# Kernel optimization log

Measured on AMD Instinct MI355X. Metric: run time of the kernel, lower is better.

Reference implementation:

```python
import jax, jax.numpy as jnp
import numpy as np

IN_CHANNELS = 8
CHANNELS = 8
MASK_OUT_STRIDE = 4


def aligned_bilinear(x, factor):
    # Faithful port of AdelaiDet aligned_bilinear (align_corners=True).
    if factor == 1:
        return x
    n, c, h, w = x.shape
    x = jnp.pad(x, ((0, 0), (0, 0), (0, 1), (0, 1)), mode='edge')
    oh, ow = factor * h + 1, factor * w + 1

    def interp_axis(arr, out_len, axis):
        # align_corners=True from size s+1 -> factor*s+1: src coord = i / factor
        coords = jnp.arange(out_len) / factor
        i0 = jnp.floor(coords).astype(jnp.int32)
        i1 = jnp.minimum(i0 + 1, arr.shape[axis] - 1)
        t = (coords - i0).astype(arr.dtype)
        a0 = jnp.take(arr, i0, axis=axis)
        a1 = jnp.take(arr, i1, axis=axis)
        shp = [1] * arr.ndim
        shp[axis] = out_len
        t = t.reshape(shp)
        return a0 * (1 - t) + a1 * t

    x = interp_axis(x, oh, 2)
    x = interp_axis(x, ow, 3)
    p = factor // 2
    x = jnp.pad(x, ((0, 0), (0, 0), (p, 0), (p, 0)), mode='edge')
    return x[:, :, : oh - 1, : ow - 1]


def setup_inputs() -> dict:
    key = jax.random.key(0)
    ks = jax.random.split(key, 6)
    N, C, H, W = 4, IN_CHANNELS, 112, 200
    n_inst = 200
    stride = 8
    num_gen_params = (C + 2) * CHANNELS + CHANNELS + CHANNELS * CHANNELS + CHANNELS + CHANNELS + 1  # 169
    mask_feats = jax.random.normal(ks[0], (N, C, H, W), dtype=jnp.float32)
    mask_head_params = jax.random.normal(ks[1], (n_inst, num_gen_params), dtype=jnp.float32) * 0.1
    # instance centers anywhere inside the image (in input-image pixel coords)
    instance_locations = jax.random.uniform(ks[2], (n_inst, 2), dtype=jnp.float32) * jnp.array(
        [W * stride, H * stride], dtype=jnp.float32)
    sizes_of_interest = jnp.array([64.0, 128.0, 256.0, 512.0, 1024.0], dtype=jnp.float32)
    im_inds = jax.random.randint(ks[3], (n_inst,), 0, N, dtype=jnp.int32)
    fpn_levels = jax.random.randint(ks[4], (n_inst,), 0, 5, dtype=jnp.int32)
    return {
        'mask_feats': mask_feats,
        'mask_head_params': mask_head_params,
        'instance_locations': instance_locations,
        'sizes_of_interest': sizes_of_interest,
        'im_inds': im_inds,
        'fpn_levels': fpn_levels,
        'mask_feat_stride': stride,
    }


def reference(mask_feats, mask_head_params, instance_locations, sizes_of_interest,
              im_inds, fpn_levels, mask_feat_stride):
    N, C, H, W = mask_feats.shape
    n_inst = mask_head_params.shape[0]
    HW = H * W
    stride = mask_feat_stride  # python int

    # compute_locations: (x, y) pairs, x fastest, at pixel centers (stride//2 offset)
    xs = (jnp.arange(W) * stride + stride // 2).astype(mask_feats.dtype)
    ys = (jnp.arange(H) * stride + stride // 2).astype(mask_feats.dtype)
    gx, gy = jnp.meshgrid(xs, ys, indexing='xy')  # [H, W]
    locations = jnp.stack([gx, gy], axis=-1).reshape(HW, 2)  # [HW, 2]

    # relative coords, normalized by size-of-interest per instance
    rel = instance_locations[:, None, :] - locations[None, :, :]  # [n, HW, 2]
    rel = jnp.transpose(rel, (0, 2, 1))  # [n, 2, HW]
    soi = sizes_of_interest[fpn_levels]  # [n]
    rel = rel / soi[:, None, None]

    feats = mask_feats[im_inds].reshape(n_inst, C, HW)  # [n, C, HW]
    x = jnp.concatenate([rel, feats], axis=1)  # [n, C+2, HW]

    # parse_dynamic_params: split [n, 169] into per-layer 1x1 conv weights/biases
    wn = [(C + 2) * CHANNELS, CHANNELS * CHANNELS, CHANNELS * 1]
    bn = [CHANNELS, CHANNELS, 1]
    sizes = wn + bn
    offs = np.cumsum([0] + sizes)
    parts = [mask_head_params[:, offs[i]:offs[i + 1]] for i in range(len(sizes))]
    w0 = parts[0].reshape(n_inst, CHANNELS, C + 2)
    w1 = parts[1].reshape(n_inst, CHANNELS, CHANNELS)
    w2 = parts[2].reshape(n_inst, 1, CHANNELS)
    b0, b1, b2 = parts[3], parts[4], parts[5]

    # per-instance grouped 1x1 convs == batched matmuls over instances
    x = jax.nn.relu(jnp.einsum('noi,nip->nop', w0, x) + b0[:, :, None])
    x = jax.nn.relu(jnp.einsum('noi,nip->nop', w1, x) + b1[:, :, None])
    x = jnp.einsum('noi,nip->nop', w2, x) + b2[:, :, None]  # [n, 1, HW]

    mask_logits = x.reshape(n_inst, 1, H, W)
    factor = stride // MASK_OUT_STRIDE
    return aligned_bilinear(mask_logits, factor)
```

## Files before the change

kernel.cpp:

```cpp
#include <hip/hip_runtime.h>


#define IN_C   8
#define CHN    8
#define Hh     112
#define Ww     200
#define HWp    (Hh * Ww)
#define OH     224
#define OW     400
#define TY     16
#define RL     9
#define NPIX   (RL * Ww)
#define NTILES (OH / TY)
#define NPARAMS 169
#define BLK    256

typedef __fp16 h2v __attribute__((ext_vector_type(2)));

__device__ __forceinline__ uint pkh(float a, float b) {
    h2v p = __builtin_amdgcn_cvt_pkrtz(a, b);
    union { h2v v; uint u; } cv; cv.v = p; return cv.u;
}
__device__ __forceinline__ float fdot2u(uint a, uint b, float c) {
    union { uint u; h2v v; } ua, ub; ua.u = a; ub.u = b;
#if __has_builtin(__builtin_amdgcn_fdot2)
    return __builtin_amdgcn_fdot2(ua.v, ub.v, c, false);
#else
    float d;
    asm("v_dot2_f32_f16 %0, %1, %2, %3" : "=v"(d) : "v"(ua.v), "v"(ub.v), "v"(c));
    return d;
#endif
}


__global__ __launch_bounds__(BLK, 8)
void dmh_fused_kernel(const float* __restrict__ feats,
                      const float* __restrict__ params,
                      const float* __restrict__ iloc,
                      const float* __restrict__ soi_tab,
                      const int*   __restrict__ im_inds,
                      const int*   __restrict__ fpn_levels,
                      float* __restrict__ out)
{
    __shared__ float bl[20];
    __shared__ float lgt[RL][Ww];

    const int bid  = blockIdx.x;
    const int inst = bid / NTILES;
    const int ty   = bid - inst * NTILES;
    const int y0   = ty * TY;
    const int r_lo = (y0 > 0 ? (y0 - 1) : 0) >> 1;
    const int tid  = threadIdx.x;

    const float* __restrict__ wp = params + inst * NPARAMS;
    if (tid < 8)       bl[tid]      = wp[152 + tid];
    else if (tid < 16) bl[tid]      = wp[160 + (tid - 8)];
    else if (tid == 16) bl[16]      = wp[168];

    uint w0p[40], w1p[32], w2p[4];
    #pragma unroll
    for (int o = 0; o < CHN; o++) {
        w0p[o * 5 + 0] = pkh(wp[o * 10 + 0], wp[o * 10 + 1]);
        #pragma unroll
        for (int j = 0; j < 4; j++)
            w0p[o * 5 + 1 + j] = pkh(wp[o * 10 + 2 + 2 * j], wp[o * 10 + 3 + 2 * j]);
    }
    #pragma unroll
    for (int o = 0; o < CHN; o++)
        #pragma unroll
        for (int j = 0; j < 4; j++)
            w1p[o * 4 + j] = pkh(wp[80 + o * 8 + 2 * j], wp[80 + o * 8 + 2 * j + 1]);
    #pragma unroll
    for (int j = 0; j < 4; j++)
        w2p[j] = pkh(wp[144 + 2 * j], wp[144 + 2 * j + 1]);

    #pragma unroll
    for (int i = 0; i < 40; i++) {
        w0p[i] = __builtin_amdgcn_readfirstlane(w0p[i]);
        asm volatile("" : "+s"(w0p[i]));
    }
    #pragma unroll
    for (int i = 0; i < 32; i++) {
        w1p[i] = __builtin_amdgcn_readfirstlane(w1p[i]);
        asm volatile("" : "+s"(w1p[i]));
    }
    #pragma unroll
    for (int i = 0; i < 4; i++) {
        w2p[i] = __builtin_amdgcn_readfirstlane(w2p[i]);
        asm volatile("" : "+s"(w2p[i]));
    }

    const float soi    = soi_tab[fpn_levels[inst]];
    const float inv_s  = 1.0f / soi;
    const float ix     = iloc[inst * 2 + 0];
    const float iy     = iloc[inst * 2 + 1];
    const float* __restrict__ fb = feats + (size_t)im_inds[inst] * (IN_C * HWp);

    __syncthreads();

    for (int p = tid; p < NPIX; p += BLK) {
        const int rr = p / Ww;
        const int c  = p - rr * Ww;
        const int r  = r_lo + rr;
        const float* fp = fb + r * Ww + c;

        uint f_pk[4];
        #pragma unroll
        for (int j = 0; j < 4; j++)
            f_pk[j] = pkh(fp[(2 * j) * HWp], fp[(2 * j + 1) * HWp]);

        const float in1 = (iy - (float)(r * 8 + 4)) * inv_s;
        const float in0 = (ix - (float)(c * 8 + 4)) * inv_s;
        const uint  in_pk = pkh(in0, in1);

        float hv[CHN];
        #pragma unroll
        for (int o = 0; o < CHN; o++) {
            float t = bl[o];
            t = fdot2u(in_pk,  w0p[o * 5 + 0], t);
            t = fdot2u(f_pk[0], w0p[o * 5 + 1], t);
            t = fdot2u(f_pk[1], w0p[o * 5 + 2], t);
            t = fdot2u(f_pk[2], w0p[o * 5 + 3], t);
            t = fdot2u(f_pk[3], w0p[o * 5 + 4], t);
            hv[o] = fmaxf(t, 0.0f);
        }
        uint h_pk[4];
        #pragma unroll
        for (int j = 0; j < 4; j++) h_pk[j] = pkh(hv[2 * j], hv[2 * j + 1]);

        float gv[CHN];
        #pragma unroll
        for (int o = 0; o < CHN; o++) {
            float a = bl[8 + o];
            a = fdot2u(h_pk[0], w1p[o * 4 + 0], a);
            a = fdot2u(h_pk[1], w1p[o * 4 + 1], a);
            a = fdot2u(h_pk[2], w1p[o * 4 + 2], a);
            a = fdot2u(h_pk[3], w1p[o * 4 + 3], a);
            gv[o] = fmaxf(a, 0.0f);
        }
        uint g_pk[4];
        #pragma unroll
        for (int j = 0; j < 4; j++) g_pk[j] = pkh(gv[2 * j], gv[2 * j + 1]);

        float r0 = bl[16];
        r0 = fdot2u(g_pk[0], w2p[0], r0);
        r0 = fdot2u(g_pk[1], w2p[1], r0);
        r0 = fdot2u(g_pk[2], w2p[2], r0);
        r0 = fdot2u(g_pk[3], w2p[3], r0);

        lgt[rr][c] = r0;
    }
    __syncthreads();

    float* __restrict__ ob = out + (size_t)inst * (OH * OW);
    const int NQ = (TY * OW) / 4;
    for (int q = tid; q < NQ; q += BLK) {
        const int dy = q / (OW / 4);
        const int gx = q - dy * (OW / 4);
        const int x  = gx * 4;
        const int y  = y0 + dy;
        const int i  = (y > 0 ? y - 1 : 0);
        const int rr0 = (i >> 1) - r_lo;
        const int r1g = (i >> 1) + (i & 1);
        const int rr1 = (r1g > Hh - 1 ? Hh - 1 : r1g) - r_lo;
        const float wy1 = (i & 1) ? 0.5f : 0.0f;
        const float wy0 = 1.0f - wy1;

        const int cx  = x >> 1;
        const int cm1 = (cx > 0 ? cx - 1 : 0);
        const float a_m = lgt[rr0][cm1], a_0 = lgt[rr0][cx], a_p = lgt[rr0][cx + 1];
        const float b_m = lgt[rr1][cm1], b_0 = lgt[rr1][cx], b_p = lgt[rr1][cx + 1];
        const float Rm = wy0 * a_m + wy1 * b_m;
        const float R0 = wy0 * a_0 + wy1 * b_0;
        const float Rp = wy0 * a_p + wy1 * b_p;

        float4 o4;
        o4.x = 0.5f * (Rm + R0);
        o4.y = R0;
        o4.z = 0.5f * (R0 + Rp);
        o4.w = Rp;
        *reinterpret_cast<float4*>(&ob[y * OW + x]) = o4;
    }
}

extern "C" void kernel_launch(void* const* d_in, const int* in_sizes, int n_in,
                              void* d_out, int out_size, void* d_ws, size_t ws_size,
                              hipStream_t stream) {
    const float* mask_feats = (const float*)d_in[0];
    const float* params     = (const float*)d_in[1];
    const float* iloc       = (const float*)d_in[2];
    const float* soi        = (const float*)d_in[3];
    const int*   im_inds    = (const int*)d_in[4];
    const int*   fpn        = (const int*)d_in[5];
    float* out = (float*)d_out;

    const int n_inst = in_sizes[4];
    dim3 grid(n_inst * NTILES);
    dim3 block(BLK);
    hipLaunchKernelGGL(dmh_fused_kernel, grid, block, 0, stream,
                       mask_feats, params, iloc, soi, im_inds, fpn, out);
}
```

Before: 48.02 us.

## Pre-pack features to fp16 in a repack pass, enlarge tiles, keep weights in VGPRs

Adds a separate kernel that converts the 8-channel fp32 feature maps into packed fp16 uint4 per pixel in workspace. The main kernel then does one 16-byte load per pixel instead of eight strided fp32 loads plus conversions. Tile height doubles to 32, which reduces the halo-row recompute and the number of blocks. Weights and biases move from SGPRs and LDS into VGPRs. The extra launch, the workspace round trip, and higher register pressure with lower occupancy (launch bounds 4) are the costs.

After: 43.70 us. 9.0% less time.

```diff
diff --git a/kernel.cpp b/kernel.cpp
--- a/kernel.cpp
+++ b/kernel.cpp
@@ -8,8 +8,8 @@
 #define HWp    (Hh * Ww)
 #define OH     224
 #define OW     400
-#define TY     16
-#define RL     9
+#define TY     32
+#define RL     17
 #define NPIX   (RL * Ww)
 #define NTILES (OH / TY)
 #define NPARAMS 169
@@ -32,9 +32,25 @@
 #endif
 }
 
-
-__global__ __launch_bounds__(BLK, 8)
-void dmh_fused_kernel(const float* __restrict__ feats,
+__global__ __launch_bounds__(BLK)
+void dmh_repack_kernel(const float* __restrict__ feats, uint4* __restrict__ fpk)
+{
+    const int p = blockIdx.x * BLK + threadIdx.x;
+    if (p >= 4 * HWp) return;
+    const int img = p / HWp;
+    const int px  = p - img * HWp;
+    const float* f = feats + (size_t)img * (IN_C * HWp) + px;
+    uint4 u;
+    u.x = pkh(f[0 * HWp], f[1 * HWp]);
+    u.y = pkh(f[2 * HWp], f[3 * HWp]);
+    u.z = pkh(f[4 * HWp], f[5 * HWp]);
+    u.w = pkh(f[6 * HWp], f[7 * HWp]);
+    fpk[p] = u;
+}
+
+
+__global__ __launch_bounds__(BLK, 4)
+void dmh_fused_kernel(const uint4* __restrict__ fpk,
                       const float* __restrict__ params,
                       const float* __restrict__ iloc,
                       const float* __restrict__ soi_tab,
@@ -42,7 +58,6 @@
                       const int*   __restrict__ fpn_levels,
                       float* __restrict__ out)
 {
-    __shared__ float bl[20];
     __shared__ float lgt[RL][Ww];
 
     const int bid  = blockIdx.x;
@@ -53,11 +68,9 @@
     const int tid  = threadIdx.x;
 
     const float* __restrict__ wp = params + inst * NPARAMS;
-    if (tid < 8)       bl[tid]      = wp[152 + tid];
-    else if (tid < 16) bl[tid]      = wp[160 + (tid - 8)];
-    else if (tid == 16) bl[16]      = wp[168];
 
     uint w0p[40], w1p[32], w2p[4];
+    float b0v[CHN], b1v[CHN], b2v;
     #pragma unroll
     for (int o = 0; o < CHN; o++) {
         w0p[o * 5 + 0] = pkh(wp[o * 10 + 0], wp[o * 10 + 1]);
@@ -73,41 +86,37 @@
     #pragma unroll
     for (int j = 0; j < 4; j++)
         w2p[j] = pkh(wp[144 + 2 * j], wp[144 + 2 * j + 1]);
-
-    #pragma unroll
-    for (int i = 0; i < 40; i++) {
-        w0p[i] = __builtin_amdgcn_readfirstlane(w0p[i]);
-        asm volatile("" : "+s"(w0p[i]));
-    }
-    #pragma unroll
-    for (int i = 0; i < 32; i++) {
-        w1p[i] = __builtin_amdgcn_readfirstlane(w1p[i]);
-        asm volatile("" : "+s"(w1p[i]));
-    }
-    #pragma unroll
-    for (int i = 0; i < 4; i++) {
-        w2p[i] = __builtin_amdgcn_readfirstlane(w2p[i]);
-        asm volatile("" : "+s"(w2p[i]));
-    }
+    #pragma unroll
+    for (int i = 0; i < CHN; i++) b0v[i] = wp[152 + i];
+    #pragma unroll
+    for (int i = 0; i < CHN; i++) b1v[i] = wp[160 + i];
+    b2v = wp[168];
+
+    #pragma unroll
+    for (int i = 0; i < 40; i++) asm volatile("" : "+v"(w0p[i]));
+    #pragma unroll
+    for (int i = 0; i < 32; i++) asm volatile("" : "+v"(w1p[i]));
+    #pragma unroll
+    for (int i = 0; i < 4; i++)  asm volatile("" : "+v"(w2p[i]));
+    #pragma unroll
+    for (int i = 0; i < CHN; i++) asm volatile("" : "+v"(b0v[i]));
+    #pragma unroll
+    for (int i = 0; i < CHN; i++) asm volatile("" : "+v"(b1v[i]));
+    asm volatile("" : "+v"(b2v));
 
     const float soi    = soi_tab[fpn_levels[inst]];
     const float inv_s  = 1.0f / soi;
     const float ix     = iloc[inst * 2 + 0];
     const float iy     = iloc[inst * 2 + 1];
-    const float* __restrict__ fb = feats + (size_t)im_inds[inst] * (IN_C * HWp);
-
-    __syncthreads();
+    const uint4* __restrict__ fb = fpk + (size_t)im_inds[inst] * HWp;
 
     for (int p = tid; p < NPIX; p += BLK) {
         const int rr = p / Ww;
         const int c  = p - rr * Ww;
         const int r  = r_lo + rr;
-        const float* fp = fb + r * Ww + c;
-
-        uint f_pk[4];
-        #pragma unroll
-        for (int j = 0; j < 4; j++)
-            f_pk[j] = pkh(fp[(2 * j) * HWp], fp[(2 * j + 1) * HWp]);
+
+        const uint4 u = fb[r * Ww + c];
+        const uint f0 = u.x, f1 = u.y, f2 = u.z, f3 = u.w;
 
         const float in1 = (iy - (float)(r * 8 + 4)) * inv_s;
         const float in0 = (ix - (float)(c * 8 + 4)) * inv_s;
@@ -116,12 +125,12 @@
         float hv[CHN];
         #pragma unroll
         for (int o = 0; o < CHN; o++) {
-            float t = bl[o];
-            t = fdot2u(in_pk,  w0p[o * 5 + 0], t);
-            t = fdot2u(f_pk[0], w0p[o * 5 + 1], t);
-            t = fdot2u(f_pk[1], w0p[o * 5 + 2], t);
-            t = fdot2u(f_pk[2], w0p[o * 5 + 3], t);
-            t = fdot2u(f_pk[3], w0p[o * 5 + 4], t);
+            float t = b0v[o];
+            t = fdot2u(in_pk, w0p[o * 5 + 0], t);
+            t = fdot2u(f0,    w0p[o * 5 + 1], t);
+            t = fdot2u(f1,    w0p[o * 5 + 2], t);
+            t = fdot2u(f2,    w0p[o * 5 + 3], t);
+            t = fdot2u(f3,    w0p[o * 5 + 4], t);
             hv[o] = fmaxf(t, 0.0f);
         }
         uint h_pk[4];
@@ -131,7 +140,7 @@
         float gv[CHN];
         #pragma unroll
         for (int o = 0; o < CHN; o++) {
-            float a = bl[8 + o];
+            float a = b1v[o];
             a = fdot2u(h_pk[0], w1p[o * 4 + 0], a);
             a = fdot2u(h_pk[1], w1p[o * 4 + 1], a);
             a = fdot2u(h_pk[2], w1p[o * 4 + 2], a);
@@ -142,7 +151,7 @@
         #pragma unroll
         for (int j = 0; j < 4; j++) g_pk[j] = pkh(gv[2 * j], gv[2 * j + 1]);
 
-        float r0 = bl[16];
+        float r0 = b2v;
         r0 = fdot2u(g_pk[0], w2p[0], r0);
         r0 = fdot2u(g_pk[1], w2p[1], r0);
         r0 = fdot2u(g_pk[2], w2p[2], r0);
@@ -193,10 +202,15 @@
     const int*   im_inds    = (const int*)d_in[4];
     const int*   fpn        = (const int*)d_in[5];
     float* out = (float*)d_out;
+    uint4* fpk = (uint4*)d_ws;
 
     const int n_inst = in_sizes[4];
-    dim3 grid(n_inst * NTILES);
-    dim3 block(BLK);
-    hipLaunchKernelGGL(dmh_fused_kernel, grid, block, 0, stream,
-                       mask_feats, params, iloc, soi, im_inds, fpn, out);
-}
+
+    dim3 g1((4 * HWp + BLK - 1) / BLK);
+    hipLaunchKernelGGL(dmh_repack_kernel, g1, dim3(BLK), 0, stream,
+                       mask_feats, fpk);
+
+    dim3 g2(n_inst * NTILES);
+    hipLaunchKernelGGL(dmh_fused_kernel, g2, dim3(BLK), 0, stream,
+                       fpk, params, iloc, soi, im_inds, fpn, out);
+}
```
